# Kernel optimization log

Measured on AMD Instinct MI355X. Metric: run time of the kernel, lower is better.

## Reference

```python
import jax, jax.numpy as jnp
import numpy as np

N, E, G = 50000, 320000, 256
BN_EPS = 1e-5
HEADS = 4


def _bn(x, g, b):
    # eval-mode BatchNorm1d with running_mean=0, running_var=1
    return g * (x * np.float32(1.0 / np.sqrt(1.0 + BN_EPS))) + b


def _mlp(x, w1, b1, w2, b2):
    return jax.nn.relu(x @ w1 + b1) @ w2 + b2


def _gatv2(x, src, dst, ea, lw, lb, rw, rb, ew, att, bias):
    n = x.shape[0]
    H = HEADS
    C = lw.shape[1] // H
    # self-loops with edge_attr = mean of incoming edge features (fill_value='mean')
    deg = jax.ops.segment_sum(jnp.ones((ea.shape[0],), x.dtype), dst, num_segments=n)
    loop_ea = jax.ops.segment_sum(ea, dst, num_segments=n) / jnp.maximum(deg, 1.0)[:, None]
    ar = jnp.arange(n)
    s = jnp.concatenate([src, ar])
    d = jnp.concatenate([dst, ar])
    ea_all = jnp.concatenate([ea, loop_ea], axis=0)
    xl = (x @ lw + lb).reshape(n, H, C)   # lin_l (source / message features)
    xr = (x @ rw + rb).reshape(n, H, C)   # lin_r (target)
    ee = (ea_all @ ew).reshape(-1, H, C)  # lin_edge (no bias)
    m = jax.nn.leaky_relu(xl[s] + xr[d] + ee, 0.2)       # [E+N, H, C]
    a = jnp.einsum('ehc,hc->eh', m, att)                 # attention logits
    amax = jax.ops.segment_max(a, d, num_segments=n)
    ex = jnp.exp(a - amax[d])
    den = jax.ops.segment_sum(ex, d, num_segments=n)
    w = ex / den[d]                                      # scatter-softmax over target
    out = jax.ops.segment_sum(xl[s] * w[..., None], d, num_segments=n)
    return out.reshape(n, H * C) + bias


def _meta(x, ea, u, src, dst, batch, ep, gp, up):
    # EdgeModel -> NodeModel(GATv2 + relu) -> GlobalModel (residuals=False, eval dropout)
    ea2 = _mlp(jnp.concatenate([x[src], x[dst], ea], axis=1), *ep)
    xn = jax.nn.relu(_gatv2(x, src, dst, ea2, *gp))
    pooled = jax.ops.segment_sum(xn, batch, num_segments=G)
    u2 = _mlp(jnp.concatenate([u, pooled], axis=1), *up)
    return xn, ea2, u2


def _forward(x, edge_attr, e1_w1, e1_b1, e1_w2, e1_b2, g1_lw, g1_lb, g1_rw, g1_rb, g1_ew, g1_att, g1_bias, u1_w1, u1_b1, u1_w2, u1_b2, bn_n_g, bn_n_b, bn_e_g, bn_e_b, bn_u_g, bn_u_b, e2_w1, e2_b1, e2_w2, e2_b2, g2_lw, g2_lb, g2_rw, g2_rb, g2_ew, g2_att, g2_bias, u2_w1, u2_b1, u2_w2, u2_b2, fc1_w, fc1_b, fc2_w, fc2_b, src, dst, batch):
    u0 = jnp.zeros((G, 256), x.dtype)
    x1, ea1, u1 = _meta(x, edge_attr, u0, src, dst, batch,
                        (e1_w1, e1_b1, e1_w2, e1_b2),
                        (g1_lw, g1_lb, g1_rw, g1_rb, g1_ew, g1_att, g1_bias),
                        (u1_w1, u1_b1, u1_w2, u1_b2))
    x1 = _bn(x1, bn_n_g, bn_n_b)
    ea1 = _bn(ea1, bn_e_g, bn_e_b)
    u1 = _bn(u1, bn_u_g, bn_u_b)
    _, _, u2 = _meta(x1, ea1, u1, src, dst, batch,
                     (e2_w1, e2_b1, e2_w2, e2_b2),
                     (g2_lw, g2_lb, g2_rw, g2_rb, g2_ew, g2_att, g2_bias),
                     (u2_w1, u2_b1, u2_w2, u2_b2))
    h = jax.nn.relu(u2 @ fc1_w + fc1_b)
    return h @ fc2_w + fc2_b


def setup_inputs() -> dict:
    key = jax.random.key(0)
    ks = iter(jax.random.split(key, 64))
    rp = lambda shape: jax.random.normal(next(ks), shape, jnp.float32) * 0.05
    inp = {}
    inp['x'] = jax.random.normal(next(ks), (N, 64), jnp.float32)
    inp['edge_attr'] = jax.random.normal(next(ks), (E, 16), jnp.float32)
    # layer 1: EdgeModel(64,16,h=64,out=128), GATv2(64->256,H=4,edge=128), Global(256+256->256)
    inp.update(e1_w1=rp((144, 64)), e1_b1=rp((64,)), e1_w2=rp((64, 128)), e1_b2=rp((128,)))
    inp.update(g1_lw=rp((64, 256)), g1_lb=rp((256,)), g1_rw=rp((64, 256)), g1_rb=rp((256,)),
               g1_ew=rp((128, 256)), g1_att=rp((4, 64)), g1_bias=rp((256,)))
    inp.update(u1_w1=rp((512, 256)), u1_b1=rp((256,)), u1_w2=rp((256, 256)), u1_b2=rp((256,)))
    inp.update(bn_n_g=jnp.ones((256,), jnp.float32), bn_n_b=jnp.zeros((256,), jnp.float32),
               bn_e_g=jnp.ones((128,), jnp.float32), bn_e_b=jnp.zeros((128,), jnp.float32),
               bn_u_g=jnp.ones((256,), jnp.float32), bn_u_b=jnp.zeros((256,), jnp.float32))
    # layer 2: EdgeModel(256,128,h=128,out=128), GATv2(256->256,H=4,edge=128), Global
    inp.update(e2_w1=rp((640, 128)), e2_b1=rp((128,)), e2_w2=rp((128, 128)), e2_b2=rp((128,)))
    inp.update(g2_lw=rp((256, 256)), g2_lb=rp((256,)), g2_rw=rp((256, 256)), g2_rb=rp((256,)),
               g2_ew=rp((128, 256)), g2_att=rp((4, 64)), g2_bias=rp((256,)))
    inp.update(u2_w1=rp((512, 256)), u2_b1=rp((256,)), u2_w2=rp((256, 256)), u2_b2=rp((256,)))
    inp.update(fc1_w=rp((256, 64)), fc1_b=rp((64,)), fc2_w=rp((64, 1)), fc2_b=rp((1,)))
    inp['edge_index'] = jax.random.randint(next(ks), (2, E), 0, N, jnp.int64)
    inp['batch'] = jnp.sort(jax.random.randint(next(ks), (N,), 0, G, jnp.int64))
    return inp


def reference(x, edge_attr, e1_w1, e1_b1, e1_w2, e1_b2, g1_lw, g1_lb, g1_rw, g1_rb, g1_ew, g1_att, g1_bias, u1_w1, u1_b1, u1_w2, u1_b2, bn_n_g, bn_n_b, bn_e_g, bn_e_b, bn_u_g, bn_u_b, e2_w1, e2_b1, e2_w2, e2_b2, g2_lw, g2_lb, g2_rw, g2_rb, g2_ew, g2_att, g2_bias, u2_w1, u2_b1, u2_w2, u2_b2, fc1_w, fc1_b, fc2_w, fc2_b, edge_index, batch):
    return _forward(x, edge_attr, e1_w1, e1_b1, e1_w2, e1_b2, g1_lw, g1_lb, g1_rw, g1_rb, g1_ew, g1_att, g1_bias, u1_w1, u1_b1, u1_w2, u1_b2, bn_n_g, bn_n_b, bn_e_g, bn_e_b, bn_u_g, bn_u_b, e2_w1, e2_b1, e2_w2, e2_b2, g2_lw, g2_lb, g2_rw, g2_rb, g2_ew, g2_att, g2_bias, u2_w1, u2_b1, u2_w2, u2_b2, fc1_w, fc1_b, fc2_w, fc2_b, edge_index[0], edge_index[1], batch)
```

## Files before the change

kernel.cpp:

```cpp
#include <hip/hip_runtime.h>
#include <hip/hip_bf16.h>
#include <hip/hip_fp8.h>
#include <cstdint>
#include <cstddef>

#define INVS 0.99999500003749968f
#define G_GRAPHS 256

using bf16 = __hip_bfloat16;
using short8 = __attribute__((ext_vector_type(8))) short;
using floatx4 = __attribute__((ext_vector_type(4))) float;

__device__ __forceinline__ unsigned short f2bf(float v) {
    union { float f; unsigned u; } x; x.f = v;
    unsigned r = x.u + 0x7fffu + ((x.u >> 16) & 1u);
    return (unsigned short)(r >> 16);
}
__device__ __forceinline__ float bfu(unsigned short u) { return __uint_as_float((unsigned)u << 16); }
__device__ __forceinline__ float fp82f(unsigned char b) {
    __hip_fp8_e4m3 q; q.__x = b; return (float)q;
}
__device__ __forceinline__ unsigned pk_bf16(float a, float b) {
    unsigned r;
    asm("v_cvt_pk_bf16_f32 %0, %1, %2" : "=v"(r) : "v"(a), "v"(b));
    return r;
}
__device__ __forceinline__ unsigned pk_fp8x4(float a, float b, float c, float d) {
#if __has_builtin(__builtin_amdgcn_cvt_pk_fp8_f32)
    int u = __builtin_amdgcn_cvt_pk_fp8_f32(a, b, 0, false);
    u = __builtin_amdgcn_cvt_pk_fp8_f32(c, d, u, true);
    return (unsigned)u;
#else
    __hip_fp8_e4m3 qa(a), qb(b), qc(c), qd(d);
    return (unsigned)qa.__x | ((unsigned)qb.__x << 8) | ((unsigned)qc.__x << 16) | ((unsigned)qd.__x << 24);
#endif
}

__global__ void degi_k(const int* __restrict__ dst, int* __restrict__ degi, int E) {
    int gid = blockIdx.x * 256 + threadIdx.x;
    if (gid < E) atomicAdd(&degi[dst[gid]], 1);
}

__global__ __launch_bounds__(1024) void scan_blk_k(const int* __restrict__ degi,
                                                   int* __restrict__ off,
                                                   int* __restrict__ bsum, int N) {
    __shared__ int buf[1024];
    int t = threadIdx.x;
    int base = blockIdx.x * 2048;
    int i0 = base + 2 * t, i1 = base + 2 * t + 1;
    int v0 = (i0 < N) ? (degi[i0] + 1) : 0;
    int v1 = (i1 < N) ? (degi[i1] + 1) : 0;
    int s = v0 + v1;
    buf[t] = s;
    __syncthreads();
    for (int ofs = 1; ofs < 1024; ofs <<= 1) {
        int add = (t >= ofs) ? buf[t - ofs] : 0;
        __syncthreads();
        buf[t] += add;
        __syncthreads();
    }
    int excl = buf[t] - s;
    if (i0 < N) off[i0] = excl;
    if (i1 < N) off[i1] = excl + v0;
    if (t == 1023) bsum[blockIdx.x] = buf[1023];
}

__global__ void scan_top_k(const int* __restrict__ bsum, int* __restrict__ boff,
                           int* __restrict__ off, int NBLK, int N) {
    if (threadIdx.x == 0 && blockIdx.x == 0) {
        int run = 0;
        for (int i = 0; i < NBLK; ++i) { boff[i] = run; run += bsum[i]; }
        off[N] = run;
    }
}

__global__ void scan_add_k(int* __restrict__ off, const int* __restrict__ boff, int N) {
    int gid = blockIdx.x * 256 + threadIdx.x;
    if (gid < N) off[gid] += boff[gid >> 11];
}

__global__ void fill_csr_k(const int* __restrict__ src, const int* __restrict__ dst,
                           const int* __restrict__ off, int* __restrict__ fillc,
                           int* __restrict__ csr_src, int* __restrict__ csr_dst,
                           int* __restrict__ csr_eid, int E, int N) {
    int gid = blockIdx.x * 256 + threadIdx.x;
    if (gid < E) {
        int d = dst[gid];
        int slot = off[d] + atomicAdd(&fillc[d], 1);
        csr_src[slot] = src[gid];
        csr_dst[slot] = d;
        csr_eid[slot] = gid;
    }
    if (gid < N) {
        int slot = off[gid + 1] - 1;
        csr_src[slot] = gid;
        csr_dst[slot] = gid;
        csr_eid[slot] = E + gid;
    }
}

__global__ void conv_weights1_k(const float* __restrict__ w1, const float* __restrict__ w2,
                                short* __restrict__ w1p, short* __restrict__ w1c,
                                short* __restrict__ w2s) {
    int gid = blockIdx.x * 256 + threadIdx.x;
    if (gid < 1024) {
        int f = gid >> 6, lane = gid & 63;
        int kk = f >> 3, tt = f & 7;
        int n = tt * 16 + (lane & 15);
        int k0 = kk * 32 + (lane >> 4) * 8;
        short8 v;
        for (int j = 0; j < 8; ++j) {
            int k = k0 + j;
            float x = (n < 64) ? w1[k * 64 + n] : w1[(64 + k) * 64 + (n - 64)];
            v[j] = (short)f2bf(x);
        }
        *(short8*)(w1p + (long long)gid * 8) = v;
    } else if (gid < 1280) {
        int g2 = gid - 1024;
        int tt = g2 >> 6, lane = g2 & 63;
        int n = tt * 16 + (lane & 15);
        int k0 = (lane >> 4) * 8;
        short8 v;
        for (int j = 0; j < 8; ++j) {
            int k = k0 + j;
            v[j] = (k < 16) ? (short)f2bf(w1[(128 + k) * 64 + n]) : (short)0;
        }
        *(short8*)(w1c + (long long)g2 * 8) = v;
    } else if (gid < 2304) {
        int g2 = gid - 1280;
        int f = g2 >> 6, lane = g2 & 63;
        int kk = f >> 3, tt = f & 7;
        int n = tt * 16 + (lane & 15);
        int k0 = kk * 32 + (lane >> 4) * 8;
        short8 v;
        for (int j = 0; j < 8; ++j) v[j] = (short)f2bf(w2[(k0 + j) * 128 + n]);
        *(short8*)(w2s + (long long)g2 * 8) = v;
    }
}

__global__ void conv_ew_k(const float* __restrict__ ew, short* __restrict__ ews) {
    int gid = blockIdx.x * 256 + threadIdx.x;
    if (gid >= 4096) return;
    int f = gid >> 6, lane = gid & 63;
    int kk = f >> 4, tt = f & 15;
    int n = tt * 16 + (lane & 15);
    int k0 = kk * 32 + (lane >> 4) * 8;
    short8 v;
    for (int j = 0; j < 8; ++j) v[j] = (short)f2bf(ew[(k0 + j) * 256 + n]);
    *(short8*)(ews + (long long)gid * 8) = v;
}

template <int K>
__global__ void conv_nodew_k(const float* __restrict__ wl, const float* __restrict__ wr,
                             short* __restrict__ out) {
    int gid = blockIdx.x * 256 + threadIdx.x;
    if (gid >= (K / 32) * 32 * 64) return;
    int f = gid >> 6, lane = gid & 63;
    int kk = f >> 5, tt = f & 31;
    int n = tt * 16 + (lane & 15);
    int k0 = kk * 32 + (lane >> 4) * 8;
    short8 v;
    for (int j = 0; j < 8; ++j) {
        int k = k0 + j;
        float x = (n < 256) ? wl[k * 256 + n] : wr[k * 256 + (n - 256)];
        v[j] = (short)f2bf(x);
    }
    *(short8*)(out + (long long)gid * 8) = v;
}

__global__ void conv_pre2w_k(const float* __restrict__ w1, short* __restrict__ out) {
    int gid = blockIdx.x * 256 + threadIdx.x;
    if (gid >= 8 * 16 * 64) return;
    int f = gid >> 6, lane = gid & 63;
    int kk = f >> 4, tt = f & 15;
    int n = tt * 16 + (lane & 15);
    int k0 = kk * 32 + (lane >> 4) * 8;
    short8 v;
    for (int j = 0; j < 8; ++j) {
        int k = k0 + j;
        float x = (n < 128) ? w1[k * 128 + n] : w1[(256 + k) * 128 + (n - 128)];
        v[j] = (short)f2bf(x);
    }
    *(short8*)(out + (long long)gid * 8) = v;
}

__global__ __launch_bounds__(256) void pre1_mfma_k(
    const float* __restrict__ x, const short* __restrict__ w1p,
    const float* __restrict__ b1, bf16* __restrict__ pre1, int N) {
    __shared__ short At[16][72];
    __shared__ short Ot[16][136];
    int t = threadIdx.x;
    long long n0 = (long long)blockIdx.x * 16;
    {
        int r = t >> 4, c = t & 15;
        long long n = n0 + r;
        float4 v = {0.f, 0.f, 0.f, 0.f};
        if (n < N) v = *(const float4*)(x + n * 64 + c * 4);
        ushort4 pk;
        pk.x = f2bf(v.x); pk.y = f2bf(v.y); pk.z = f2bf(v.z); pk.w = f2bf(v.w);
        *(ushort4*)&At[r][c * 4] = pk;
    }
    __syncthreads();
    int w = t >> 6, lane = t & 63;
    int nq = w * 2;
    int lr = lane & 15, lq = lane >> 4;
    floatx4 acc[2];
    for (int i = 0; i < 2; ++i) acc[i] = (floatx4){0.f, 0.f, 0.f, 0.f};
    for (int kk = 0; kk < 2; ++kk) {
        short8 a = *(const short8*)&At[lr][kk * 32 + lq * 8];
        for (int tt = 0; tt < 2; ++tt) {
            short8 b = *(const short8*)(w1p + ((long long)((kk * 8 + nq + tt) * 64 + lane)) * 8);
            acc[tt] = __builtin_amdgcn_mfma_f32_16x16x32_bf16(a, b, acc[tt], 0, 0, 0);
        }
    }
    for (int tt = 0; tt < 2; ++tt) {
        int col = (nq + tt) * 16 + lr;
        float bv = (col >= 64) ? b1[col - 64] : 0.f;
        for (int r = 0; r < 4; ++r)
            Ot[lq * 4 + r][col] = (short)f2bf(acc[tt][r] + bv);
    }
    __syncthreads();
    {
        int r = t >> 4, c = t & 15;
        long long n = n0 + r;
        if (n < N)
            *(short8*)(void*)(pre1 + n * 128 + c * 8) = *(const short8*)&Ot[r][c * 8];
    }
}

__global__ __launch_bounds__(256) void edge_mlp1_mfma_k(
    const bf16* __restrict__ pre1, const float* __restrict__ ea,
    const int* __restrict__ csr_src, const int* __restrict__ csr_dst,
    const int* __restrict__ csr_eid,
    const short* __restrict__ w1c,
    const short* __restrict__ w2s, const float* __restrict__ b2,
    const short* __restrict__ ews,
    unsigned char* __restrict__ ee8, int NT, int E) {
    __shared__ float Ps[32][76];
    __shared__ short Ae[32][40];
    __shared__ short Ht[32][72];
    __shared__ short A2[32][136];
    __shared__ int sdv[32][3];
    unsigned char* Et = (unsigned char*)&Ps[0][0];
    int t = threadIdx.x;
    long long s0 = (long long)blockIdx.x * 32;
    if (t < 96) {
        int r = t & 31, which = t >> 5;
        long long s = s0 + r;
        int v = (which == 2) ? E : 0;
        if (s < NT) v = (which == 0) ? csr_src[s] : (which == 1 ? csr_dst[s] : csr_eid[s]);
        sdv[r][which] = v;
    }
    __syncthreads();
    {
        int r = t >> 3, c = t & 7;
        long long s = s0 + r;
        bool ok = (s < NT) && (sdv[r][2] < E);
        float p[8];
        if (ok) {
            short8 vs = *(const short8*)(const void*)(pre1 + (long long)sdv[r][0] * 128 + c * 8);
            short8 vd = *(const short8*)(const void*)(pre1 + (long long)sdv[r][1] * 128 + 64 + c * 8);
            for (int j = 0; j < 8; ++j)
                p[j] = bfu((unsigned short)vs[j]) + bfu((unsigned short)vd[j]);
        } else {
            for (int j = 0; j < 8; ++j) p[j] = 0.f;
        }
        for (int j = 0; j < 8; ++j) Ps[r][c * 8 + j] = p[j];
    }
    if (t < 128) {
        int r = t >> 2, c = t & 3;
        long long s = s0 + r;
        int eid = sdv[r][2];
        float4 v = {0.f, 0.f, 0.f, 0.f};
        if (s < NT && eid < E) v = *(const float4*)(ea + (long long)eid * 16 + c * 4);
        ushort4 pk;
        pk.x = f2bf(v.x); pk.y = f2bf(v.y); pk.z = f2bf(v.z); pk.w = f2bf(v.w);
        *(ushort4*)&Ae[r][c * 4] = pk;
    } else {
        int i = t - 128;
        int r = i >> 2, c = i & 3;
        *(ushort4*)&Ae[r][16 + c * 4] = (ushort4){0, 0, 0, 0};
    }
    __syncthreads();

    int w = t >> 6, lane = t & 63;
    int sl = (w & 1) * 16 + (lane & 15);
    int lq = lane >> 4;

    {
        int mb = (w >> 1) * 2;
        floatx4 acc[2];
        #pragma unroll
        for (int tt = 0; tt < 2; ++tt)
            acc[tt] = *(const floatx4*)&Ps[sl][(mb + tt) * 16 + lq * 4];
        short8 bfr = *(const short8*)&Ae[sl][lq * 8];
        #pragma unroll
        for (int tt = 0; tt < 2; ++tt) {
            short8 a = *(const short8*)(w1c + ((long long)((mb + tt) * 64 + lane)) * 8);
            acc[tt] = __builtin_amdgcn_mfma_f32_16x16x32_bf16(a, bfr, acc[tt], 0, 0, 0);
        }
        #pragma unroll
        for (int tt = 0; tt < 2; ++tt) {
            int ch0 = (mb + tt) * 16 + lq * 4;
            uint2 o;
            o.x = pk_bf16(fmaxf(acc[tt][0], 0.f), fmaxf(acc[tt][1], 0.f));
            o.y = pk_bf16(fmaxf(acc[tt][2], 0.f), fmaxf(acc[tt][3], 0.f));
            *(uint2*)&Ht[sl][ch0] = o;
        }
    }
    __syncthreads();

    {
        int mb = (w >> 1) * 4;
        floatx4 acc2[4];
        #pragma unroll
        for (int i = 0; i < 4; ++i) acc2[i] = (floatx4){0.f, 0.f, 0.f, 0.f};
        #pragma unroll
        for (int kk = 0; kk < 2; ++kk) {
            short8 bfr = *(const short8*)&Ht[sl][kk * 32 + lq * 8];
            #pragma unroll
            for (int tt = 0; tt < 4; ++tt) {
                short8 a = *(const short8*)(w2s + ((long long)((kk * 8 + mb + tt) * 64 + lane)) * 8);
                acc2[tt] = __builtin_amdgcn_mfma_f32_16x16x32_bf16(a, bfr, acc2[tt], 0, 0, 0);
            }
        }
        #pragma unroll
        for (int tt = 0; tt < 4; ++tt) {
            int ch0 = (mb + tt) * 16 + lq * 4;
            float4 bv = *(const float4*)(b2 + ch0);
            uint2 o;
            o.x = pk_bf16(acc2[tt][0] + bv.x, acc2[tt][1] + bv.y);
            o.y = pk_bf16(acc2[tt][2] + bv.z, acc2[tt][3] + bv.w);
            *(uint2*)&A2[sl][ch0] = o;
        }
    }
    __syncthreads();

    {
        int mb = (w >> 1) * 8;
        floatx4 acc3[8];
        #pragma unroll
        for (int i = 0; i < 8; ++i) acc3[i] = (floatx4){0.f, 0.f, 0.f, 0.f};
        #pragma unroll
        for (int kk = 0; kk < 4; ++kk) {
            short8 bfr = *(const short8*)&A2[sl][kk * 32 + lq * 8];
            #pragma unroll
            for (int tt = 0; tt < 8; ++tt) {
                short8 a = *(const short8*)(ews + ((long long)((kk * 16 + mb + tt) * 64 + lane)) * 8);
                acc3[tt] = __builtin_amdgcn_mfma_f32_16x16x32_bf16(a, bfr, acc3[tt], 0, 0, 0);
            }
        }
        #pragma unroll
        for (int tt = 0; tt < 8; ++tt) {
            int ch0 = (mb + tt) * 16 + lq * 4;
            unsigned u = pk_fp8x4(acc3[tt][0], acc3[tt][1], acc3[tt][2], acc3[tt][3]);
            *(unsigned*)(Et + sl * 272 + ch0) = u;
        }
    }
    __syncthreads();
    for (int i = t; i < 512; i += 256) {
        int r = i >> 4, c = i & 15;
        long long s = s0 + r;
        if (s < NT)
            *(uint4*)(ee8 + s * 256 + c * 16) = *(const uint4*)(Et + r * 272 + c * 16);
    }
}

template <int K, typename T>
__global__ __launch_bounds__(256) void node_linear_mfma_k(
    const T* x, const short* __restrict__ ws,
    const float* __restrict__ bl, const float* __restrict__ br,
    bf16* __restrict__ xl, bf16* xr, int N) {
    __shared__ short At[16][K + 8];
    __shared__ short Ot[16][520];
    int t = threadIdx.x;
    long long n0 = (long long)blockIdx.x * 16;
    if (sizeof(T) == 4) {
        for (int i = t; i < 16 * (K / 4); i += 256) {
            int r = i / (K / 4), c = i % (K / 4);
            long long n = n0 + r;
            float4 v = {0.f, 0.f, 0.f, 0.f};
            if (n < N) v = *(const float4*)((const float*)x + n * K + c * 4);
            ushort4 pk;
            pk.x = f2bf(v.x); pk.y = f2bf(v.y); pk.z = f2bf(v.z); pk.w = f2bf(v.w);
            *(ushort4*)&At[r][c * 4] = pk;
        }
    } else {
        for (int i = t; i < 16 * (K / 8); i += 256) {
            int r = i / (K / 8), c = i % (K / 8);
            long long n = n0 + r;
            short8 v = {0, 0, 0, 0, 0, 0, 0, 0};
            if (n < N) v = *(const short8*)(const void*)((const bf16*)x + n * K + c * 8);
            *(short8*)&At[r][c * 8] = v;
        }
    }
    __syncthreads();

    int w = t >> 6, lane = t & 63;
    int nr = lane & 15, lq = lane >> 4;

    floatx4 acc[8];
    #pragma unroll
    for (int i = 0; i < 8; ++i) acc[i] = (floatx4){0.f, 0.f, 0.f, 0.f};
    for (int kk = 0; kk < K / 32; ++kk) {
        short8 bfr = *(const short8*)&At[nr][kk * 32 + lq * 8];
        #pragma unroll
        for (int tt = 0; tt < 8; ++tt) {
            short8 a = *(const short8*)(ws + ((long long)((kk * 32 + w * 8 + tt) * 64 + lane)) * 8);
            acc[tt] = __builtin_amdgcn_mfma_f32_16x16x32_bf16(a, bfr, acc[tt], 0, 0, 0);
        }
    }
    #pragma unroll
    for (int tt = 0; tt < 8; ++tt) {
        int ch0 = (w * 8 + tt) * 16 + lq * 4;
        const float* bp = (ch0 < 256) ? (bl + ch0) : (br + (ch0 - 256));
        float4 bv = *(const float4*)bp;
        uint2 o;
        o.x = pk_bf16(acc[tt][0] + bv.x, acc[tt][1] + bv.y);
        o.y = pk_bf16(acc[tt][2] + bv.z, acc[tt][3] + bv.w);
        *(uint2*)&Ot[nr][ch0] = o;
    }
    __syncthreads();
    for (int i = t; i < 1024; i += 256) {
        int r = i >> 6, c = i & 63;
        long long n = n0 + r;
        if (n < N) {
            short8 v = *(const short8*)&Ot[r][c * 8];
            if (c < 32) *(short8*)(void*)(xl + n * 256 + c * 8) = v;
            else        *(short8*)(void*)(xr + n * 256 + (c - 32) * 8) = v;
        }
    }
}

__global__ __launch_bounds__(256) void pre_mfma_k(
    const bf16* __restrict__ x, const short* __restrict__ ws,
    const float* __restrict__ bx, bf16* __restrict__ out, int N) {
    __shared__ short At[16][264];
    __shared__ short Ot[16][264];
    int t = threadIdx.x;
    long long n0 = (long long)blockIdx.x * 16;
    for (int i = t; i < 512; i += 256) {
        int r = i >> 5, c = i & 31;
        long long n = n0 + r;
        short8 v = {0, 0, 0, 0, 0, 0, 0, 0};
        if (n < N) v = *(const short8*)(const void*)(x + n * 256 + c * 8);
        *(short8*)&At[r][c * 8] = v;
    }
    __syncthreads();

    int w = t >> 6, lane = t & 63;
    int nr = lane & 15, lq = lane >> 4;

    floatx4 acc[4];
    #pragma unroll
    for (int i = 0; i < 4; ++i) acc[i] = (floatx4){0.f, 0.f, 0.f, 0.f};
    for (int kk = 0; kk < 8; ++kk) {
        short8 bfr = *(const short8*)&At[nr][kk * 32 + lq * 8];
        #pragma unroll
        for (int tt = 0; tt < 4; ++tt) {
            short8 a = *(const short8*)(ws + ((long long)((kk * 16 + w * 4 + tt) * 64 + lane)) * 8);
            acc[tt] = __builtin_amdgcn_mfma_f32_16x16x32_bf16(a, bfr, acc[tt], 0, 0, 0);
        }
    }
    #pragma unroll
    for (int tt = 0; tt < 4; ++tt) {
        int ch0 = (w * 4 + tt) * 16 + lq * 4;
        float4 bv = *(const float4*)(bx + ch0);
        uint2 o;
        o.x = pk_bf16(acc[tt][0] + bv.x, acc[tt][1] + bv.y);
        o.y = pk_bf16(acc[tt][2] + bv.z, acc[tt][3] + bv.w);
        *(uint2*)&Ot[nr][ch0] = o;
    }
    __syncthreads();
    for (int i = t; i < 512; i += 256) {
        int r = i >> 5, c = i & 31;
        long long n = n0 + r;
        if (n < N)
            *(short8*)(void*)(out + n * 256 + c * 8) = *(const short8*)&Ot[r][c * 8];
    }
}

template <bool L1>
__global__ __launch_bounds__(256) void gat_fused_k(
    const unsigned char* __restrict__ ee8, const bf16* __restrict__ xl, const bf16* xr,
    const int* __restrict__ off, const int* __restrict__ csr_src,
    const float* __restrict__ att, const float* __restrict__ bias,
    const float* __restrict__ bng, const float* __restrict__ bnb,
    const int* __restrict__ batch,
    bf16* x1bn, float* __restrict__ pooled, int N) {
    __shared__ float ps[4][260];
    __shared__ int bid[4];
    int t = threadIdx.x;
    int w = t >> 6, lane = t & 63;
    int n = blockIdx.x * 4 + w;
    bool valid = n < N;
    int c0 = lane * 4;
    float o0 = 0.f, o1 = 0.f, o2 = 0.f, o3 = 0.f;
    if (valid) {
        ushort4 xrp = *(const ushort4*)(const void*)(xr + (long long)n * 256 + c0);
        ushort4 xop = *(const ushort4*)(const void*)(xl + (long long)n * 256 + c0);
        float xr0 = bfu(xrp.x), xr1 = bfu(xrp.y), xr2 = bfu(xrp.z), xr3 = bfu(xrp.w);
        float4 atv = *(const float4*)(att + c0);
        float a0 = 0.f, a1 = 0.f, a2 = 0.f, a3 = 0.f, dacc = 0.f;
        float es0 = 0.f, es1 = 0.f, es2 = 0.f, es3 = 0.f;
        int beg = off[n], end1 = off[n + 1] - 1;
        ushort4 xlp;
        unsigned ep;
        {
            int sid = csr_src[beg];
            xlp = *(const ushort4*)(const void*)(xl + (long long)sid * 256 + c0);
            ep = *(const unsigned*)(ee8 + (long long)beg * 256 + c0);
        }
        for (int i = beg; i < end1; ++i) {
            ushort4 cx = xlp;
            unsigned ce = ep;
            if (i + 1 < end1) {
                int sid = csr_src[i + 1];
                xlp = *(const ushort4*)(const void*)(xl + (long long)sid * 256 + c0);
                ep = *(const unsigned*)(ee8 + (long long)(i + 1) * 256 + c0);
            }
            float x0 = bfu(cx.x), x1 = bfu(cx.y), x2 = bfu(cx.z), x3 = bfu(cx.w);
            float e0 = fp82f(ce & 0xff);
            float e1 = fp82f((ce >> 8) & 0xff);
            float e2 = fp82f((ce >> 16) & 0xff);
            float e3 = fp82f(ce >> 24);
            es0 += e0; es1 += e1; es2 += e2; es3 += e3;
            float m0 = x0 + xr0 + e0;
            float m1 = x1 + xr1 + e1;
            float m2 = x2 + xr2 + e2;
            float m3 = x3 + xr3 + e3;
            m0 = m0 > 0.f ? m0 : 0.2f * m0;
            m1 = m1 > 0.f ? m1 : 0.2f * m1;
            m2 = m2 > 0.f ? m2 : 0.2f * m2;
            m3 = m3 > 0.f ? m3 : 0.2f * m3;
            float p = atv.x * m0 + atv.y * m1 + atv.z * m2 + atv.w * m3;
            p += __shfl_xor(p, 1, 64);
            p += __shfl_xor(p, 2, 64);
            p += __shfl_xor(p, 4, 64);
            p += __shfl_xor(p, 8, 64);
            float ex = expf(p);
            a0 += ex * x0; a1 += ex * x1; a2 += ex * x2; a3 += ex * x3;
            dacc += ex;
        }
        {
            float rdv = 1.f / fmaxf((float)(end1 - beg), 1.f);
            float x0 = bfu(xop.x), x1 = bfu(xop.y), x2 = bfu(xop.z), x3 = bfu(xop.w);
            float m0 = x0 + xr0 + es0 * rdv;
            float m1 = x1 + xr1 + es1 * rdv;
            float m2 = x2 + xr2 + es2 * rdv;
            float m3 = x3 + xr3 + es3 * rdv;
            m0 = m0 > 0.f ? m0 : 0.2f * m0;
            m1 = m1 > 0.f ? m1 : 0.2f * m1;
            m2 = m2 > 0.f ? m2 : 0.2f * m2;
            m3 = m3 > 0.f ? m3 : 0.2f * m3;
            float p = atv.x * m0 + atv.y * m1 + atv.z * m2 + atv.w * m3;
            p += __shfl_xor(p, 1, 64);
            p += __shfl_xor(p, 2, 64);
            p += __shfl_xor(p, 4, 64);
            p += __shfl_xor(p, 8, 64);
            float ex = expf(p);
            a0 += ex * x0; a1 += ex * x1; a2 += ex * x2; a3 += ex * x3;
            dacc += ex;
        }
        float inv = 1.f / dacc;
        o0 = fmaxf(a0 * inv + bias[c0],     0.f);
        o1 = fmaxf(a1 * inv + bias[c0 + 1], 0.f);
        o2 = fmaxf(a2 * inv + bias[c0 + 2], 0.f);
        o3 = fmaxf(a3 * inv + bias[c0 + 3], 0.f);
        if (L1) {
            ushort4 o;
            o.x = f2bf(bng[c0]     * (o0 * INVS) + bnb[c0]);
            o.y = f2bf(bng[c0 + 1] * (o1 * INVS) + bnb[c0 + 1]);
            o.z = f2bf(bng[c0 + 2] * (o2 * INVS) + bnb[c0 + 2]);
            o.w = f2bf(bng[c0 + 3] * (o3 * INVS) + bnb[c0 + 3]);
            *(ushort4*)(void*)(x1bn + (long long)n * 256 + c0) = o;
        }
    }
    if (lane == 0) bid[w] = valid ? batch[n] : -1;
    ps[w][c0]     = o0;
    ps[w][c0 + 1] = o1;
    ps[w][c0 + 2] = o2;
    ps[w][c0 + 3] = o3;
    __syncthreads();
    int b0 = bid[0];
    bool same = (b0 >= 0)
             && (bid[1] < 0 || bid[1] == b0)
             && (bid[2] < 0 || bid[2] == b0)
             && (bid[3] < 0 || bid[3] == b0);
    if (same) {
        float s = ps[0][t] + ps[1][t] + ps[2][t] + ps[3][t];
        atomicAdd(&pooled[(long long)b0 * 256 + t], s);
    } else if (valid) {
        long long pb = (long long)bid[w] * 256 + c0;
        atomicAdd(&pooled[pb],     o0);
        atomicAdd(&pooled[pb + 1], o1);
        atomicAdd(&pooled[pb + 2], o2);
        atomicAdd(&pooled[pb + 3], o3);
    }
}

__global__ void global_mlp1_k(const float* __restrict__ pooled,
                              const float* __restrict__ w1, const float* __restrict__ b1,
                              const float* __restrict__ w2, const float* __restrict__ b2,
                              const float* __restrict__ bng, const float* __restrict__ bnb,
                              float* __restrict__ u1bn) {
    __shared__ float pr[256];
    __shared__ float h[256];
    int t = threadIdx.x, g = blockIdx.x;
    pr[t] = pooled[g * 256 + t];
    __syncthreads();
    float acc = b1[t];
    for (int k = 0; k < 256; ++k) acc += pr[k] * w1[(256 + k) * 256 + t];
    h[t] = fmaxf(acc, 0.f);
    __syncthreads();
    float a2 = b2[t];
    for (int k = 0; k < 256; ++k) a2 += h[k] * w2[k * 256 + t];
    u1bn[g * 256 + t] = bng[t] * (a2 * INVS) + bnb[t];
}

__global__ void conv_weights_k(const float* __restrict__ w1, const float* __restrict__ w2,
                               const float* __restrict__ b1,
                               const float* __restrict__ bg, const float* __restrict__ bb,
                               short* __restrict__ w1s, short* __restrict__ w2s,
                               float* __restrict__ b1x) {
    int gid = blockIdx.x * 256 + threadIdx.x;
    if (gid < 10240) {
        int f = gid >> 6, lane = gid & 63;
        int kk = f >> 3, tt = f & 7;
        int n = tt * 16 + (lane & 15);
        int k0 = kk * 32 + (lane >> 4) * 8;
        short8 v;
        for (int j = 0; j < 8; ++j) {
            int k = k0 + j;
            float x = w1[k * 128 + n];
            if (k >= 512) x *= bg[k - 512] * INVS;
            v[j] = (short)f2bf(x);
        }
        *(short8*)(w1s + (long long)gid * 8) = v;
    } else if (gid < 12288) {
        int g2 = gid - 10240;
        int f = g2 >> 6, lane = g2 & 63;
        int kk = f >> 3, tt = f & 7;
        int n = tt * 16 + (lane & 15);
        int k0 = kk * 32 + (lane >> 4) * 8;
        short8 v;
        for (int j = 0; j < 8; ++j) v[j] = (short)f2bf(w2[(k0 + j) * 128 + n]);
        *(short8*)(w2s + (long long)g2 * 8) = v;
    } else if (gid < 12544) {
        int j = gid - 12288;
        b1x[j] = 0.f;
    } else if (gid < 12672) {
        int j = gid - 12544;
        float acc = b1[j];
        for (int c = 0; c < 128; ++c) acc += bb[c] * w1[(512 + c) * 128 + j];
        b1x[128 + j] = acc;
    }
}

__global__ __launch_bounds__(256) void edge_mlp2_mfma_k(
    const bf16* __restrict__ xpre, const bf16* __restrict__ pre1,
    const float* __restrict__ ea,
    const int* __restrict__ csr_src, const int* __restrict__ csr_dst,
    const int* __restrict__ csr_eid,
    const short* __restrict__ w1c, const short* __restrict__ w2s1,
    const float* __restrict__ e1_b2,
    const short* __restrict__ w1s,
    const short* __restrict__ w2s, const float* __restrict__ b2,
    const short* __restrict__ ews,
    unsigned char* __restrict__ ee8, int NT, int E) {
    __shared__ float Ps[32][140];
    __shared__ short At[32][136];
    __shared__ short Ht[32][136];
    __shared__ short Ae[32][40];
    __shared__ int sdv[32][3];
    unsigned char* Et = (unsigned char*)&Ps[0][0];
    int t = threadIdx.x;
    long long s0 = (long long)blockIdx.x * 32;
    if (t < 96) {
        int r = t & 31, which = t >> 5;
        long long s = s0 + r;
        int v = (which == 2) ? E : 0;
        if (s < NT) v = (which == 0) ? csr_src[s] : (which == 1 ? csr_dst[s] : csr_eid[s]);
        sdv[r][which] = v;
    }
    __syncthreads();
    {
        int r = t >> 3, c = t & 7;
        long long s = s0 + r;
        bool ok = (s < NT) && (sdv[r][2] < E);
        float p[8];
        if (ok) {
            short8 vs = *(const short8*)(const void*)(pre1 + (long long)sdv[r][0] * 128 + c * 8);
            short8 vd = *(const short8*)(const void*)(pre1 + (long long)sdv[r][1] * 128 + 64 + c * 8);
            for (int j = 0; j < 8; ++j)
                p[j] = bfu((unsigned short)vs[j]) + bfu((unsigned short)vd[j]);
        } else {
            for (int j = 0; j < 8; ++j) p[j] = 0.f;
        }
        for (int j = 0; j < 8; ++j) Ps[r][c * 8 + j] = p[j];
    }
    if (t < 128) {
        int r = t >> 2, c = t & 3;
        long long s = s0 + r;
        int eid = sdv[r][2];
        float4 v = {0.f, 0.f, 0.f, 0.f};
        if (s < NT && eid < E) v = *(const float4*)(ea + (long long)eid * 16 + c * 4);
        ushort4 pk;
        pk.x = f2bf(v.x); pk.y = f2bf(v.y); pk.z = f2bf(v.z); pk.w = f2bf(v.w);
        *(ushort4*)&Ae[r][c * 4] = pk;
    } else {
        int i = t - 128;
        int r = i >> 2, c = i & 3;
        *(ushort4*)&Ae[r][16 + c * 4] = (ushort4){0, 0, 0, 0};
    }
    __syncthreads();

    int w = t >> 6, lane = t & 63;
    int sl = (w & 1) * 16 + (lane & 15);
    int lq = lane >> 4;

    {
        int mb = (w >> 1) * 2;
        floatx4 acc[2];
        #pragma unroll
        for (int tt = 0; tt < 2; ++tt)
            acc[tt] = *(const floatx4*)&Ps[sl][(mb + tt) * 16 + lq * 4];
        short8 bfr = *(const short8*)&Ae[sl][lq * 8];
        #pragma unroll
        for (int tt = 0; tt < 2; ++tt) {
            short8 a = *(const short8*)(w1c + ((long long)((mb + tt) * 64 + lane)) * 8);
            acc[tt] = __builtin_amdgcn_mfma_f32_16x16x32_bf16(a, bfr, acc[tt], 0, 0, 0);
        }
        #pragma unroll
        for (int tt = 0; tt < 2; ++tt) {
            int ch0 = (mb + tt) * 16 + lq * 4;
            uint2 o;
            o.x = pk_bf16(fmaxf(acc[tt][0], 0.f), fmaxf(acc[tt][1], 0.f));
            o.y = pk_bf16(fmaxf(acc[tt][2], 0.f), fmaxf(acc[tt][3], 0.f));
            *(uint2*)&Ht[sl][ch0] = o;
        }
    }
    __syncthreads();

    for (int i = t; i < 512; i += 256) {
        int r = i >> 4, c = i & 15;
        long long s = s0 + r;
        bool ok = (s < NT) && (sdv[r][2] < E);
        float p[8];
        if (ok) {
            short8 vs = *(const short8*)(const void*)(xpre + (long long)sdv[r][0] * 256 + c * 8);
            short8 vd = *(const short8*)(const void*)(xpre + (long long)sdv[r][1] * 256 + 128 + c * 8);
            for (int j = 0; j < 8; ++j)
                p[j] = bfu((unsigned short)vs[j]) + bfu((unsigned short)vd[j]);
        } else {
            for (int j = 0; j < 8; ++j) p[j] = 0.f;
        }
        for (int j = 0; j < 8; ++j) Ps[r][c * 8 + j] = p[j];
    }
    {
        int mb = (w >> 1) * 4;
        floatx4 acc2[4];
        #pragma unroll
        for (int i = 0; i < 4; ++i) acc2[i] = (floatx4){0.f, 0.f, 0.f, 0.f};
        #pragma unroll
        for (int kk = 0; kk < 2; ++kk) {
            short8 bfr = *(const short8*)&Ht[sl][kk * 32 + lq * 8];
            #pragma unroll
            for (int tt = 0; tt < 4; ++tt) {
                short8 a = *(const short8*)(w2s1 + ((long long)((kk * 8 + mb + tt) * 64 + lane)) * 8);
                acc2[tt] = __builtin_amdgcn_mfma_f32_16x16x32_bf16(a, bfr, acc2[tt], 0, 0, 0);
            }
        }
        #pragma unroll
        for (int tt = 0; tt < 4; ++tt) {
            int ch0 = (mb + tt) * 16 + lq * 4;
            float4 bv = *(const float4*)(e1_b2 + ch0);
            uint2 o;
            o.x = pk_bf16(acc2[tt][0] + bv.x, acc2[tt][1] + bv.y);
            o.y = pk_bf16(acc2[tt][2] + bv.z, acc2[tt][3] + bv.w);
            *(uint2*)&At[sl][ch0] = o;
        }
    }
    __syncthreads();

    {
        int mb = (w >> 1) * 4;
        floatx4 acc[4];
        #pragma unroll
        for (int tt = 0; tt < 4; ++tt)
            acc[tt] = *(const floatx4*)&Ps[sl][(mb + tt) * 16 + lq * 4];
        #pragma unroll
        for (int kk = 0; kk < 4; ++kk) {
            short8 bfr = *(const short8*)&At[sl][kk * 32 + lq * 8];
            #pragma unroll
            for (int tt = 0; tt < 4; ++tt) {
                short8 a = *(const short8*)(w1s + ((long long)(((16 + kk) * 8 + mb + tt) * 64 + lane)) * 8);
                acc[tt] = __builtin_amdgcn_mfma_f32_16x16x32_bf16(a, bfr, acc[tt], 0, 0, 0);
            }
        }
        #pragma unroll
        for (int tt = 0; tt < 4; ++tt) {
            int ch0 = (mb + tt) * 16 + lq * 4;
            uint2 o;
            o.x = pk_bf16(fmaxf(acc[tt][0], 0.f), fmaxf(acc[tt][1], 0.f));
            o.y = pk_bf16(fmaxf(acc[tt][2], 0.f), fmaxf(acc[tt][3], 0.f));
            *(uint2*)&Ht[sl][ch0] = o;
        }
    }
    __syncthreads();

    {
        int mb = (w >> 1) * 4;
        floatx4 acc2[4];
        #pragma unroll
        for (int i = 0; i < 4; ++i) acc2[i] = (floatx4){0.f, 0.f, 0.f, 0.f};
        #pragma unroll
        for (int kk = 0; kk < 4; ++kk) {
            short8 bfr = *(const short8*)&Ht[sl][kk * 32 + lq * 8];
            #pragma unroll
            for (int tt = 0; tt < 4; ++tt) {
                short8 a = *(const short8*)(w2s + ((long long)((kk * 8 + mb + tt) * 64 + lane)) * 8);
                acc2[tt] = __builtin_amdgcn_mfma_f32_16x16x32_bf16(a, bfr, acc2[tt], 0, 0, 0);
            }
        }
        #pragma unroll
        for (int tt = 0; tt < 4; ++tt) {
            int ch0 = (mb + tt) * 16 + lq * 4;
            float4 bv = *(const float4*)(b2 + ch0);
            uint2 o;
            o.x = pk_bf16(acc2[tt][0] + bv.x, acc2[tt][1] + bv.y);
            o.y = pk_bf16(acc2[tt][2] + bv.z, acc2[tt][3] + bv.w);
            *(uint2*)&At[sl][ch0] = o;
        }
    }
    __syncthreads();

    {
        int mb = (w >> 1) * 8;
        floatx4 acc3[8];
        #pragma unroll
        for (int i = 0; i < 8; ++i) acc3[i] = (floatx4){0.f, 0.f, 0.f, 0.f};
        #pragma unroll
        for (int kk = 0; kk < 4; ++kk) {
            short8 bfr = *(const short8*)&At[sl][kk * 32 + lq * 8];
            #pragma unroll
            for (int tt = 0; tt < 8; ++tt) {
                short8 a = *(const short8*)(ews + ((long long)((kk * 16 + mb + tt) * 64 + lane)) * 8);
                acc3[tt] = __builtin_amdgcn_mfma_f32_16x16x32_bf16(a, bfr, acc3[tt], 0, 0, 0);
            }
        }
        #pragma unroll
        for (int tt = 0; tt < 8; ++tt) {
            int ch0 = (mb + tt) * 16 + lq * 4;
            unsigned u = pk_fp8x4(acc3[tt][0], acc3[tt][1], acc3[tt][2], acc3[tt][3]);
            *(unsigned*)(Et + sl * 272 + ch0) = u;
        }
    }
    __syncthreads();
    for (int i = t; i < 512; i += 256) {
        int r = i >> 4, c = i & 15;
        long long s = s0 + r;
        if (s < NT && sdv[r][2] < E)
            *(uint4*)(ee8 + s * 256 + c * 16) = *(const uint4*)(Et + r * 272 + c * 16);
    }
}

__global__ void final_mlp_k(const float* __restrict__ u1bn, const float* __restrict__ pooled,
                            const float* __restrict__ w1, const float* __restrict__ b1,
                            const float* __restrict__ w2, const float* __restrict__ b2,
                            const float* __restrict__ f1w, const float* __restrict__ f1b,
                            const float* __restrict__ f2w, const float* __restrict__ f2b,
                            float* __restrict__ out) {
    __shared__ float ub[256], pb[256], h[256], u2[256];
    int t = threadIdx.x, g = blockIdx.x;
    ub[t] = u1bn[g * 256 + t];
    pb[t] = pooled[g * 256 + t];
    __syncthreads();
    float acc = b1[t];
    for (int k = 0; k < 256; ++k)
        acc += ub[k] * w1[k * 256 + t] + pb[k] * w1[(256 + k) * 256 + t];
    h[t] = fmaxf(acc, 0.f);
    __syncthreads();
    float a2 = b2[t];
    for (int k = 0; k < 256; ++k) a2 += h[k] * w2[k * 256 + t];
    u2[t] = a2;
    __syncthreads();
    float fv = 0.f;
    if (t < 64) {
        float a3 = f1b[t];
        for (int k = 0; k < 256; ++k) a3 += u2[k] * f1w[k * 64 + t];
        fv = fmaxf(a3, 0.f) * f2w[t];
    }
    for (int off = 32; off; off >>= 1) fv += __shfl_down(fv, off, 64);
    if (t == 0) out[g] = fv + f2b[0];
}

extern "C" void kernel_launch(void* const* d_in, const int* in_sizes, int n_in,
                              void* d_out, int out_size, void* d_ws, size_t ws_size,
                              hipStream_t stream) {
    const float* x         = (const float*)d_in[0];
    const float* edge_attr = (const float*)d_in[1];
    const float* e1_w1 = (const float*)d_in[2];
    const float* e1_b1 = (const float*)d_in[3];
    const float* e1_w2 = (const float*)d_in[4];
    const float* e1_b2 = (const float*)d_in[5];
    const float* g1_lw = (const float*)d_in[6];
    const float* g1_lb = (const float*)d_in[7];
    const float* g1_rw = (const float*)d_in[8];
    const float* g1_rb = (const float*)d_in[9];
    const float* g1_ew = (const float*)d_in[10];
    const float* g1_att = (const float*)d_in[11];
    const float* g1_bias = (const float*)d_in[12];
    const float* u1_w1 = (const float*)d_in[13];
    const float* u1_b1 = (const float*)d_in[14];
    const float* u1_w2 = (const float*)d_in[15];
    const float* u1_b2 = (const float*)d_in[16];
    const float* bn_n_g = (const float*)d_in[17];
    const float* bn_n_b = (const float*)d_in[18];
    const float* bn_e_g = (const float*)d_in[19];
    const float* bn_e_b = (const float*)d_in[20];
    const float* bn_u_g = (const float*)d_in[21];
    const float* bn_u_b = (const float*)d_in[22];
    const float* e2_w1 = (const float*)d_in[23];
    const float* e2_b1 = (const float*)d_in[24];
    const float* e2_w2 = (const float*)d_in[25];
    const float* e2_b2 = (const float*)d_in[26];
    const float* g2_lw = (const float*)d_in[27];
    const float* g2_lb = (const float*)d_in[28];
    const float* g2_rw = (const float*)d_in[29];
    const float* g2_rb = (const float*)d_in[30];
    const float* g2_ew = (const float*)d_in[31];
    const float* g2_att = (const float*)d_in[32];
    const float* g2_bias = (const float*)d_in[33];
    const float* u2_w1 = (const float*)d_in[34];
    const float* u2_b1 = (const float*)d_in[35];
    const float* u2_w2 = (const float*)d_in[36];
    const float* u2_b2 = (const float*)d_in[37];
    const float* fc1_w = (const float*)d_in[38];
    const float* fc1_b = (const float*)d_in[39];
    const float* fc2_w = (const float*)d_in[40];
    const float* fc2_b = (const float*)d_in[41];
    const int* edge_index = (const int*)d_in[42];
    const int* batch = (const int*)d_in[43];

    const int N = in_sizes[0] / 64;
    const int E = in_sizes[1] / 16;
    const int NT = E + N;
    const int G = G_GRAPHS;
    const int* src = edge_index;
    const int* dst = edge_index + E;
    const int NB = (NT + 31) / 32;
    const int NSB = (N + 2047) / 2048;

    char* p = (char*)d_ws;
    auto alloc = [&](size_t bytes) { char* r = p; p += (bytes + 255) & ~(size_t)255; return r; };
    bf16* xl    = (bf16*)alloc((size_t)N * 256 * 2);
    bf16* xr    = (bf16*)alloc((size_t)N * 256 * 2);
    bf16* x1bn  = xr;
    unsigned char* ee8 = (unsigned char*)alloc((size_t)NT * 256);
    bf16* pre1  = (bf16*)alloc((size_t)N * 128 * 2);
    int* degi   = (int*)alloc((size_t)N * 4);
    int* off    = (int*)alloc((size_t)(N + 1) * 4);
    int* fillc  = (int*)alloc((size_t)N * 4);
    int* csr_src = (int*)alloc((size_t)NT * 4);
    int* csr_dst = (int*)alloc((size_t)NT * 4);
    int* csr_eid = (int*)alloc((size_t)NT * 4);
    int* bsum   = (int*)alloc((size_t)(NSB + 1) * 4);
    int* boff   = (int*)alloc((size_t)(NSB + 1) * 4);
    float* pooled = (float*)alloc((size_t)G * 256 * 4);
    float* u1bn = (float*)alloc((size_t)G * 256 * 4);
    short* w1s  = (short*)alloc((size_t)20 * 8 * 64 * 8 * 2);
    short* w2s  = (short*)alloc((size_t)4 * 8 * 64 * 8 * 2);
    float* b1x  = (float*)alloc((size_t)256 * 4);
    short* w1p  = (short*)alloc((size_t)16 * 64 * 8 * 2);
    short* w1c  = (short*)alloc((size_t)4 * 64 * 8 * 2);
    short* w2s1 = (short*)alloc((size_t)16 * 64 * 8 * 2);
    short* ews1 = (short*)alloc((size_t)4 * 16 * 64 * 8 * 2);
    short* ews2 = (short*)alloc((size_t)4 * 16 * 64 * 8 * 2);
    short* nw1  = (short*)alloc((size_t)2 * 32 * 64 * 8 * 2);
    short* nw2  = (short*)alloc((size_t)8 * 32 * 64 * 8 * 2);
    short* nwp  = (short*)alloc((size_t)8 * 16 * 64 * 8 * 2);

    hipMemsetAsync(degi, 0, (size_t)N * 4, stream);
    hipMemsetAsync(fillc, 0, (size_t)N * 4, stream);
    hipMemsetAsync(pooled, 0, (size_t)G * 256 * 4, stream);
    degi_k<<<(E + 255) / 256, 256, 0, stream>>>(dst, degi, E);
    scan_blk_k<<<NSB, 1024, 0, stream>>>(degi, off, bsum, N);
    scan_top_k<<<1, 64, 0, stream>>>(bsum, boff, off, NSB, N);
    scan_add_k<<<(N + 255) / 256, 256, 0, stream>>>(off, boff, N);
    fill_csr_k<<<(max(E, N) + 255) / 256, 256, 0, stream>>>(src, dst, off, fillc,
                                                            csr_src, csr_dst, csr_eid, E, N);

    conv_weights1_k<<<9, 256, 0, stream>>>(e1_w1, e1_w2, w1p, w1c, w2s1);
    conv_ew_k<<<16, 256, 0, stream>>>(g1_ew, ews1);
    conv_ew_k<<<16, 256, 0, stream>>>(g2_ew, ews2);
    conv_nodew_k<64><<<16, 256, 0, stream>>>(g1_lw, g1_rw, nw1);
    conv_nodew_k<256><<<64, 256, 0, stream>>>(g2_lw, g2_rw, nw2);
    conv_pre2w_k<<<32, 256, 0, stream>>>(e2_w1, nwp);
    pre1_mfma_k<<<(N + 15) / 16, 256, 0, stream>>>(x, w1p, e1_b1, pre1, N);
    edge_mlp1_mfma_k<<<NB, 256, 0, stream>>>(pre1, edge_attr, csr_src, csr_dst, csr_eid,
                                             w1c, w2s1, e1_b2, ews1, ee8, NT, E);
    node_linear_mfma_k<64, float><<<(N + 15) / 16, 256, 0, stream>>>(x, nw1, g1_lb, g1_rb, xl, xr, N);
    gat_fused_k<true><<<(N + 3) / 4, 256, 0, stream>>>(ee8, xl, xr, off, csr_src,
                                                       g1_att, g1_bias, bn_n_g, bn_n_b,
                                                       batch, x1bn, pooled, N);
    global_mlp1_k<<<G, 256, 0, stream>>>(pooled, u1_w1, u1_b1, u1_w2, u1_b2, bn_u_g, bn_u_b, u1bn);

    conv_weights_k<<<50, 256, 0, stream>>>(e2_w1, e2_w2, e2_b1, bn_e_g, bn_e_b, w1s, w2s, b1x);
    pre_mfma_k<<<(N + 15) / 16, 256, 0, stream>>>(x1bn, nwp, b1x, xl, N);
    edge_mlp2_mfma_k<<<NB, 256, 0, stream>>>(xl, pre1, edge_attr, csr_src, csr_dst, csr_eid,
                                             w1c, w2s1, e1_b2, w1s, w2s, e2_b2, ews2,
                                             ee8, NT, E);
    node_linear_mfma_k<256, bf16><<<(N + 15) / 16, 256, 0, stream>>>(x1bn, nw2, g2_lb, g2_rb, xl, xr, N);
    hipMemsetAsync(pooled, 0, (size_t)G * 256 * 4, stream);
    gat_fused_k<false><<<(N + 3) / 4, 256, 0, stream>>>(ee8, xl, xr, off, csr_src,
                                                        g2_att, g2_bias, nullptr, nullptr,
                                                        batch, nullptr, pooled, N);
    final_mlp_k<<<G, 256, 0, stream>>>(u1bn, pooled, u2_w1, u2_b1, u2_w2, u2_b2,
                                       fc1_w, fc1_b, fc2_w, fc2_b, (float*)d_out);
}
```

Baseline: 759.0 us.

## Gather edge-MLP inputs directly into MFMA registers, dropping LDS staging buffers

Both edge-MLP kernels now load the gathered src/dst pre-activation sums and the edge-attribute fragment straight from global memory into the MFMA accumulator and B-operand registers. This removes the Ps/Ae shared-memory staging, one barrier, and the LDS round trip. In edge_mlp2 the fp8 output buffer now aliases Ht, and extra __syncthreads are added so that in-place overwrites of At/Ht stay safe. The change cuts LDS footprint, which may raise occupancy, but the global loads become narrower 8-byte per-lane gathers and ea rows are converted with a different bf16 rounding helper.

```diff
diff --git a/kernel.cpp b/kernel.cpp
--- a/kernel.cpp
+++ b/kernel.cpp
@@ -236,12 +236,10 @@
     const short* __restrict__ w2s, const float* __restrict__ b2,
     const short* __restrict__ ews,
     unsigned char* __restrict__ ee8, int NT, int E) {
-    __shared__ float Ps[32][76];
-    __shared__ short Ae[32][40];
     __shared__ short Ht[32][72];
     __shared__ short A2[32][136];
+    __shared__ unsigned EtU[32][68];
     __shared__ int sdv[32][3];
-    unsigned char* Et = (unsigned char*)&Ps[0][0];
     int t = threadIdx.x;
     long long s0 = (long long)blockIdx.x * 32;
     if (t < 96) {
@@ -252,52 +250,37 @@
         sdv[r][which] = v;
     }
     __syncthreads();
-    {
-        int r = t >> 3, c = t & 7;
-        long long s = s0 + r;
-        bool ok = (s < NT) && (sdv[r][2] < E);
-        float p[8];
-        if (ok) {
-            short8 vs = *(const short8*)(const void*)(pre1 + (long long)sdv[r][0] * 128 + c * 8);
-            short8 vd = *(const short8*)(const void*)(pre1 + (long long)sdv[r][1] * 128 + 64 + c * 8);
-            for (int j = 0; j < 8; ++j)
-                p[j] = bfu((unsigned short)vs[j]) + bfu((unsigned short)vd[j]);
-        } else {
-            for (int j = 0; j < 8; ++j) p[j] = 0.f;
-        }
-        for (int j = 0; j < 8; ++j) Ps[r][c * 8 + j] = p[j];
-    }
-    if (t < 128) {
-        int r = t >> 2, c = t & 3;
-        long long s = s0 + r;
-        int eid = sdv[r][2];
-        float4 v = {0.f, 0.f, 0.f, 0.f};
-        if (s < NT && eid < E) v = *(const float4*)(ea + (long long)eid * 16 + c * 4);
-        ushort4 pk;
-        pk.x = f2bf(v.x); pk.y = f2bf(v.y); pk.z = f2bf(v.z); pk.w = f2bf(v.w);
-        *(ushort4*)&Ae[r][c * 4] = pk;
-    } else {
-        int i = t - 128;
-        int r = i >> 2, c = i & 3;
-        *(ushort4*)&Ae[r][16 + c * 4] = (ushort4){0, 0, 0, 0};
-    }
-    __syncthreads();
 
     int w = t >> 6, lane = t & 63;
     int sl = (w & 1) * 16 + (lane & 15);
     int lq = lane >> 4;
+    int srcn = sdv[sl][0], dstn = sdv[sl][1], eid = sdv[sl][2];
+
+    short8 eafr = (short8){0, 0, 0, 0, 0, 0, 0, 0};
+    if (lq < 2 && eid < E) {
+        float4 v0 = *(const float4*)(ea + (long long)eid * 16 + lq * 8);
+        float4 v1 = *(const float4*)(ea + (long long)eid * 16 + lq * 8 + 4);
+        union { uint4 u; short8 s; } cv;
+        cv.u.x = pk_bf16(v0.x, v0.y); cv.u.y = pk_bf16(v0.z, v0.w);
+        cv.u.z = pk_bf16(v1.x, v1.y); cv.u.w = pk_bf16(v1.z, v1.w);
+        eafr = cv.s;
+    }
 
     {
         int mb = (w >> 1) * 2;
         floatx4 acc[2];
         #pragma unroll
-        for (int tt = 0; tt < 2; ++tt)
-            acc[tt] = *(const floatx4*)&Ps[sl][(mb + tt) * 16 + lq * 4];
-        short8 bfr = *(const short8*)&Ae[sl][lq * 8];
+        for (int tt = 0; tt < 2; ++tt) {
+            int ch0 = (mb + tt) * 16 + lq * 4;
+            ushort4 vs = *(const ushort4*)(const void*)(pre1 + (long long)srcn * 128 + ch0);
+            ushort4 vd = *(const ushort4*)(const void*)(pre1 + (long long)dstn * 128 + 64 + ch0);
+            acc[tt] = (floatx4){bfu(vs.x) + bfu(vd.x), bfu(vs.y) + bfu(vd.y),
+                                bfu(vs.z) + bfu(vd.z), bfu(vs.w) + bfu(vd.w)};
+        }
         #pragma unroll
         for (int tt = 0; tt < 2; ++tt) {
             short8 a = *(const short8*)(w1c + ((long long)((mb + tt) * 64 + lane)) * 8);
-            acc[tt] = __builtin_amdgcn_mfma_f32_16x16x32_bf16(a, bfr, acc[tt], 0, 0, 0);
+            acc[tt] = __builtin_amdgcn_mfma_f32_16x16x32_bf16(a, eafr, acc[tt], 0, 0, 0);
         }
         #pragma unroll
         for (int tt = 0; tt < 2; ++tt) {
@@ -352,9 +335,7 @@
         }
         #pragma unroll
         for (int tt = 0; tt < 8; ++tt) {
-            int ch0 = (mb + tt) * 16 + lq * 4;
-            unsigned u = pk_fp8x4(acc3[tt][0], acc3[tt][1], acc3[tt][2], acc3[tt][3]);
-            *(unsigned*)(Et + sl * 272 + ch0) = u;
+            EtU[sl][(mb + tt) * 4 + lq] = pk_fp8x4(acc3[tt][0], acc3[tt][1], acc3[tt][2], acc3[tt][3]);
         }
     }
     __syncthreads();
@@ -362,7 +343,7 @@
         int r = i >> 4, c = i & 15;
         long long s = s0 + r;
         if (s < NT)
-            *(uint4*)(ee8 + s * 256 + c * 16) = *(const uint4*)(Et + r * 272 + c * 16);
+            *(uint4*)(ee8 + s * 256 + c * 16) = *(const uint4*)&EtU[r][c * 4];
     }
 }
 
@@ -668,12 +649,10 @@
     const short* __restrict__ w2s, const float* __restrict__ b2,
     const short* __restrict__ ews,
     unsigned char* __restrict__ ee8, int NT, int E) {
-    __shared__ float Ps[32][140];
     __shared__ short At[32][136];
     __shared__ short Ht[32][136];
-    __shared__ short Ae[32][40];
     __shared__ int sdv[32][3];
-    unsigned char* Et = (unsigned char*)&Ps[0][0];
+    unsigned char* Et = (unsigned char*)&Ht[0][0];
     int t = threadIdx.x;
     long long s0 = (long long)blockIdx.x * 32;
     if (t < 96) {
@@ -684,52 +663,37 @@
         sdv[r][which] = v;
     }
     __syncthreads();
-    {
-        int r = t >> 3, c = t & 7;
-        long long s = s0 + r;
-        bool ok = (s < NT) && (sdv[r][2] < E);
-        float p[8];
-        if (ok) {
-            short8 vs = *(const short8*)(const void*)(pre1 + (long long)sdv[r][0] * 128 + c * 8);
-            short8 vd = *(const short8*)(const void*)(pre1 + (long long)sdv[r][1] * 128 + 64 + c * 8);
-            for (int j = 0; j < 8; ++j)
-                p[j] = bfu((unsigned short)vs[j]) + bfu((unsigned short)vd[j]);
-        } else {
-            for (int j = 0; j < 8; ++j) p[j] = 0.f;
-        }
-        for (int j = 0; j < 8; ++j) Ps[r][c * 8 + j] = p[j];
-    }
-    if (t < 128) {
-        int r = t >> 2, c = t & 3;
-        long long s = s0 + r;
-        int eid = sdv[r][2];
-        float4 v = {0.f, 0.f, 0.f, 0.f};
-        if (s < NT && eid < E) v = *(const float4*)(ea + (long long)eid * 16 + c * 4);
-        ushort4 pk;
-        pk.x = f2bf(v.x); pk.y = f2bf(v.y); pk.z = f2bf(v.z); pk.w = f2bf(v.w);
-        *(ushort4*)&Ae[r][c * 4] = pk;
-    } else {
-        int i = t - 128;
-        int r = i >> 2, c = i & 3;
-        *(ushort4*)&Ae[r][16 + c * 4] = (ushort4){0, 0, 0, 0};
-    }
-    __syncthreads();
 
     int w = t >> 6, lane = t & 63;
     int sl = (w & 1) * 16 + (lane & 15);
     int lq = lane >> 4;
+    int srcn = sdv[sl][0], dstn = sdv[sl][1], eid = sdv[sl][2];
+
+    short8 eafr = (short8){0, 0, 0, 0, 0, 0, 0, 0};
+    if (lq < 2 && eid < E) {
+        float4 v0 = *(const float4*)(ea + (long long)eid * 16 + lq * 8);
+        float4 v1 = *(const float4*)(ea + (long long)eid * 16 + lq * 8 + 4);
+        union { uint4 u; short8 s; } cv;
+        cv.u.x = pk_bf16(v0.x, v0.y); cv.u.y = pk_bf16(v0.z, v0.w);
+        cv.u.z = pk_bf16(v1.x, v1.y); cv.u.w = pk_bf16(v1.z, v1.w);
+        eafr = cv.s;
+    }
 
     {
         int mb = (w >> 1) * 2;
         floatx4 acc[2];
         #pragma unroll
-        for (int tt = 0; tt < 2; ++tt)
-            acc[tt] = *(const floatx4*)&Ps[sl][(mb + tt) * 16 + lq * 4];
-        short8 bfr = *(const short8*)&Ae[sl][lq * 8];
+        for (int tt = 0; tt < 2; ++tt) {
+            int ch0 = (mb + tt) * 16 + lq * 4;
+            ushort4 vs = *(const ushort4*)(const void*)(pre1 + (long long)srcn * 128 + ch0);
+            ushort4 vd = *(const ushort4*)(const void*)(pre1 + (long long)dstn * 128 + 64 + ch0);
+            acc[tt] = (floatx4){bfu(vs.x) + bfu(vd.x), bfu(vs.y) + bfu(vd.y),
+                                bfu(vs.z) + bfu(vd.z), bfu(vs.w) + bfu(vd.w)};
+        }
         #pragma unroll
         for (int tt = 0; tt < 2; ++tt) {
             short8 a = *(const short8*)(w1c + ((long long)((mb + tt) * 64 + lane)) * 8);
-            acc[tt] = __builtin_amdgcn_mfma_f32_16x16x32_bf16(a, bfr, acc[tt], 0, 0, 0);
+            acc[tt] = __builtin_amdgcn_mfma_f32_16x16x32_bf16(a, eafr, acc[tt], 0, 0, 0);
         }
         #pragma unroll
         for (int tt = 0; tt < 2; ++tt) {
@@ -742,21 +706,6 @@
     }
     __syncthreads();
 
-    for (int i = t; i < 512; i += 256) {
-        int r = i >> 4, c = i & 15;
-        long long s = s0 + r;
-        bool ok = (s < NT) && (sdv[r][2] < E);
-        float p[8];
-        if (ok) {
-            short8 vs = *(const short8*)(const void*)(xpre + (long long)sdv[r][0] * 256 + c * 8);
-            short8 vd = *(const short8*)(const void*)(xpre + (long long)sdv[r][1] * 256 + 128 + c * 8);
-            for (int j = 0; j < 8; ++j)
-                p[j] = bfu((unsigned short)vs[j]) + bfu((unsigned short)vd[j]);
-        } else {
-            for (int j = 0; j < 8; ++j) p[j] = 0.f;
-        }
-        for (int j = 0; j < 8; ++j) Ps[r][c * 8 + j] = p[j];
-    }
     {
         int mb = (w >> 1) * 4;
         floatx4 acc2[4];
@@ -787,8 +736,13 @@
         int mb = (w >> 1) * 4;
         floatx4 acc[4];
         #pragma unroll
-        for (int tt = 0; tt < 4; ++tt)
-            acc[tt] = *(const floatx4*)&Ps[sl][(mb + tt) * 16 + lq * 4];
+        for (int tt = 0; tt < 4; ++tt) {
+            int ch0 = (mb + tt) * 16 + lq * 4;
+            ushort4 vs = *(const ushort4*)(const void*)(xpre + (long long)srcn * 256 + ch0);
+            ushort4 vd = *(const ushort4*)(const void*)(xpre + (long long)dstn * 256 + 128 + ch0);
+            acc[tt] = (floatx4){bfu(vs.x) + bfu(vd.x), bfu(vs.y) + bfu(vd.y),
+                                bfu(vs.z) + bfu(vd.z), bfu(vs.w) + bfu(vd.w)};
+        }
         #pragma unroll
         for (int kk = 0; kk < 4; ++kk) {
             short8 bfr = *(const short8*)&At[sl][kk * 32 + lq * 8];
@@ -798,6 +752,7 @@
                 acc[tt] = __builtin_amdgcn_mfma_f32_16x16x32_bf16(a, bfr, acc[tt], 0, 0, 0);
             }
         }
+        __syncthreads();
         #pragma unroll
         for (int tt = 0; tt < 4; ++tt) {
             int ch0 = (mb + tt) * 16 + lq * 4;
@@ -823,6 +778,7 @@
                 acc2[tt] = __builtin_amdgcn_mfma_f32_16x16x32_bf16(a, bfr, acc2[tt], 0, 0, 0);
             }
         }
+        __syncthreads();
         #pragma unroll
         for (int tt = 0; tt < 4; ++tt) {
             int ch0 = (mb + tt) * 16 + lq * 4;
@@ -852,8 +808,7 @@
         #pragma unroll
         for (int tt = 0; tt < 8; ++tt) {
             int ch0 = (mb + tt) * 16 + lq * 4;
-            unsigned u = pk_fp8x4(acc3[tt][0], acc3[tt][1], acc3[tt][2], acc3[tt][3]);
-            *(unsigned*)(Et + sl * 272 + ch0) = u;
+            *(unsigned*)(Et + sl * 272 + ch0) = pk_fp8x4(acc3[tt][0], acc3[tt][1], acc3[tt][2], acc3[tt][3]);
         }
     }
     __syncthreads();
```

After: 793.9 us. +4.6%, slower.
